# Kernel optimization log

Hardware: AMD Instinct MI355X
Metric: run time of the kernel (lower is better)

## Reference

```python
import jax, jax.numpy as jnp
import numpy as np

DT = 0.03125                                   # ray-march step size
NSTEPS = int(np.ceil(2.0 * np.sqrt(3.0) / DT)) # enough steps to cross the [-1,1]^3 cube diagonal (=111)


def trilinear_sample(vol, pos):
    """vol: [C, D, Hv, Wv]; pos: [H, W, 3] xyz in [-1,1] (grid_sample convention,
    align_corners=True). Returns [C, H, W]."""
    D, Hv, Wv = vol.shape[1], vol.shape[2], vol.shape[3]

    def axis(g, n):
        g = jnp.clip((g + 1.0) * 0.5 * (n - 1), 0.0, n - 1.0)
        i0 = jnp.minimum(jnp.floor(g).astype(jnp.int32), n - 2)
        return i0, i0 + 1, (g - i0)[None]  # frac broadcast over channel dim

    x0, x1, fx = axis(pos[..., 0], Wv)
    y0, y1, fy = axis(pos[..., 1], Hv)
    z0, z1, fz = axis(pos[..., 2], D)

    def g(z, y, x):
        return vol[:, z, y, x]  # [C, H, W]

    c00 = g(z0, y0, x0) * (1 - fx) + g(z0, y0, x1) * fx
    c01 = g(z0, y1, x0) * (1 - fx) + g(z0, y1, x1) * fx
    c10 = g(z1, y0, x0) * (1 - fx) + g(z1, y0, x1) * fx
    c11 = g(z1, y1, x0) * (1 - fx) + g(z1, y1, x1) * fx
    c0 = c00 * (1 - fy) + c01 * fy
    c1 = c10 * (1 - fy) + c11 * fy
    return c0 * (1 - fz) + c1 * fz


def setup_inputs() -> dict:
    key = jax.random.key(0)
    B, H, W, D = 2, 256, 256, 128
    camrot = jnp.tile(jnp.eye(3, dtype=jnp.float32)[None], (B, 1, 1))
    campos = jnp.tile(jnp.array([[0.0, 0.0, -2.5]], dtype=jnp.float32), (B, 1))
    focal = jnp.full((B, 2), 300.0, dtype=jnp.float32)
    princpt = jnp.full((B, 2), 128.0, dtype=jnp.float32)
    ys, xs = jnp.meshgrid(jnp.arange(H, dtype=jnp.float32),
                          jnp.arange(W, dtype=jnp.float32), indexing='ij')
    pixelcoords = jnp.tile(jnp.stack([xs, ys], axis=-1)[None], (B, 1, 1, 1))
    volume = jax.random.uniform(key, (B, 4, D, D, D), dtype=jnp.float32)
    return dict(camrot=camrot, campos=campos, focal=focal, princpt=princpt,
                pixelcoords=pixelcoords, volume=volume)


def reference(camrot, campos, focal, princpt, pixelcoords, volume):
    # camera rays: pixel -> camera -> world (camrot^T applied, as in torch sum over dim=-2)
    raydir = (pixelcoords - princpt[:, None, None, :]) / focal[:, None, None, :]
    raydir = jnp.concatenate([raydir, jnp.ones_like(raydir[..., :1])], axis=-1)
    raydir = jnp.einsum('bij,bhwi->bhwj', camrot, raydir)
    raydir = raydir / jnp.sqrt(jnp.sum(raydir ** 2, axis=-1, keepdims=True))

    # ray-AABB intersection with [-1,1]^3 (no grad, as in torch.no_grad())
    t1 = (-1.0 - campos[:, None, None, :]) / raydir
    t2 = (1.0 - campos[:, None, None, :]) / raydir
    tmin = jnp.maximum(jnp.minimum(t1[..., 0], t2[..., 0]),
                       jnp.maximum(jnp.minimum(t1[..., 1], t2[..., 1]),
                                   jnp.minimum(t1[..., 2], t2[..., 2])))
    tmax = jnp.minimum(jnp.maximum(t1[..., 0], t2[..., 0]),
                       jnp.minimum(jnp.maximum(t1[..., 1], t2[..., 1]),
                                   jnp.maximum(t1[..., 2], t2[..., 2])))
    hit = tmin < tmax
    t0 = jax.lax.stop_gradient(jnp.maximum(jnp.where(hit, tmin, 0.0), 0.0))

    raypos = campos[:, None, None, :] + raydir * t0[..., None]  # [B,H,W,3]
    B, H, W = raypos.shape[:3]
    rayrgb = jnp.zeros((B, 3, H, W), raypos.dtype)
    rayalpha = jnp.zeros((B, 1, H, W), raypos.dtype)

    def step(carry, _):
        raypos, rayrgb, rayalpha = carry
        valid = jnp.all((raypos > -1.0) & (raypos < 1.0), axis=-1).astype(raypos.dtype)
        samp = jax.vmap(trilinear_sample)(volume, raypos)  # [B,4,H,W]
        contrib = (jnp.minimum(rayalpha + samp[:, 3:4] * DT, 1.0) - rayalpha) * valid[:, None]
        rayrgb = rayrgb + samp[:, :3] * contrib
        rayalpha = rayalpha + contrib
        raypos = raypos + raydir * DT
        return (raypos, rayrgb, rayalpha), None

    (_, rayrgb, rayalpha), _ = jax.lax.scan(step, (raypos, rayrgb, rayalpha),
                                            None, length=NSTEPS)
    return jnp.concatenate([rayrgb, rayalpha], axis=1)  # [B,4,H,W]
```

## Files before the change

kernel.cpp:

```cpp
#include <hip/hip_runtime.h>
#include <math.h>

#pragma clang fp contract(off)

#define DT 0.03125f
#define INV_DT 32.0f
#define NSTEPS 111


__device__ __forceinline__ unsigned q8(float v) {
    return __float2uint_rn(fminf(fmaxf(v, 0.0f), 1.0f) * 255.0f);
}

__device__ __forceinline__ float chan_u8(unsigned dA, unsigned dB,
                                         float fx, float fy, float fz) {
#pragma clang fp contract(fast)
    float a00 = (float)(dA & 0xffu);
    float a10 = (float)((dA >> 8) & 0xffu);
    float a01 = (float)((dA >> 16) & 0xffu);
    float a11 = (float)((dA >> 24) & 0xffu);
    float l0 = a00 + fx * (a10 - a00);
    float l1 = a01 + fx * (a11 - a01);
    float la = l0 + fy * (l1 - l0);
    float b00 = (float)(dB & 0xffu);
    float b10 = (float)((dB >> 8) & 0xffu);
    float b01 = (float)((dB >> 16) & 0xffu);
    float b11 = (float)((dB >> 24) & 0xffu);
    float m0 = b00 + fx * (b10 - b00);
    float m1 = b01 + fx * (b11 - b01);
    float lb = m0 + fy * (m1 - m0);
    return la + fz * (lb - la);
}

__device__ __forceinline__ float4 sample_u8(uint4 A, uint4 B,
                                            float fx, float fy, float fz) {
#pragma clang fp contract(fast)
    const float s = 1.0f / 255.0f;
    float4 r;
    r.x = chan_u8(A.x, B.x, fx, fy, fz) * s;
    r.y = chan_u8(A.y, B.y, fx, fy, fz) * s;
    r.z = chan_u8(A.z, B.z, fx, fy, fz) * s;
    r.w = chan_u8(A.w, B.w, fx, fy, fz) * s;
    return r;
}

__global__ __launch_bounds__(256) void repack_u8x4_kernel(const float* __restrict__ vol,
                                                          uint4* __restrict__ out,
                                                          long spatial, int D) {
    long chunk = (long)blockIdx.x * blockDim.x + threadIdx.x;
    long nchunks = spatial >> 2;
    if (chunk >= nchunks) return;
    long b = blockIdx.y;
    long s = chunk << 2;
    int zs = D * D;
    int z = (int)(s / zs);
    int rem = (int)(s - (long)z * zs);
    int y = rem / D;
    int x0 = rem - y * D;
    int y1 = (y < D - 1) ? y + 1 : y;

    const float* base = vol + b * 4 * spatial;
    uint4 e[4];
    #pragma unroll
    for (int ci = 0; ci < 4; ++ci) {
        const float* pa = base + (long)ci * spatial + (long)z * zs + y * D + x0;
        const float* pb = base + (long)ci * spatial + (long)z * zs + y1 * D + x0;
        float4 va = *(const float4*)pa;
        float4 vb = *(const float4*)pb;
        bool last = (x0 + 4 >= D);
        float na = last ? pa[3] : pa[4];
        float nb = last ? pb[3] : pb[4];
        float ra[5] = {va.x, va.y, va.z, va.w, na};
        float rb[5] = {vb.x, vb.y, vb.z, vb.w, nb};
        #pragma unroll
        for (int k = 0; k < 4; ++k) {
            unsigned d = q8(ra[k]) | (q8(ra[k + 1]) << 8) |
                         (q8(rb[k]) << 16) | (q8(rb[k + 1]) << 24);
            ((unsigned*)&e[k])[ci] = d;
        }
    }
    uint4* o = out + b * spatial + s;
    o[0] = e[0]; o[1] = e[1]; o[2] = e[2]; o[3] = e[3];
}

__global__ __launch_bounds__(256) void repack_u8_kernel(const float* __restrict__ vol,
                                                        uint4* __restrict__ out,
                                                        long total, long spatial, int D) {
    long idx = (long)blockIdx.x * blockDim.x + threadIdx.x;
    if (idx >= total) return;
    long b = idx / spatial;
    long s = idx - b * spatial;
    int zs = D * D;
    int z = (int)(s / zs);
    int rem = (int)(s - (long)z * zs);
    int y = rem / D;
    int x = rem - y * D;
    int x1 = (x < D - 1) ? x + 1 : x;
    int y1 = (y < D - 1) ? y + 1 : y;
    const float* base = vol + b * 4 * spatial;
    uint4 e;
    #pragma unroll
    for (int ci = 0; ci < 4; ++ci) {
        const float* p = base + (long)ci * spatial + (long)z * zs;
        unsigned d = q8(p[y * D + x]) | (q8(p[y * D + x1]) << 8) |
                     (q8(p[y1 * D + x]) << 16) | (q8(p[y1 * D + x1]) << 24);
        ((unsigned*)&e)[ci] = d;
    }
    out[idx] = e;
}


struct Ray {
    float posx, posy, posz;
    float stx, sty, stz;
    int n;
};

__device__ __forceinline__ Ray ray_setup(const float* __restrict__ camrot,
                                         const float* __restrict__ campos,
                                         const float* __restrict__ focal,
                                         const float* __restrict__ princpt,
                                         const float* __restrict__ pixelcoords,
                                         int b, int y, int x, int H, int W) {
#pragma clang fp contract(off)
    long pidx = (((long)b * H + y) * W + x) * 2;
    float px = pixelcoords[pidx];
    float py = pixelcoords[pidx + 1];
    const float* R = camrot + b * 9;
    float cpx = campos[b * 3 + 0], cpy = campos[b * 3 + 1], cpz = campos[b * 3 + 2];
    float flx = focal[b * 2 + 0], fly = focal[b * 2 + 1];
    float prx = princpt[b * 2 + 0], pry = princpt[b * 2 + 1];

    float rx = (px - prx) / flx;
    float ry = (py - pry) / fly;
    float rz = 1.0f;
    float dx = R[0] * rx + R[3] * ry + R[6] * rz;
    float dy = R[1] * rx + R[4] * ry + R[7] * rz;
    float dz = R[2] * rx + R[5] * ry + R[8] * rz;
    float ss = dx * dx;
    ss = ss + dy * dy;
    ss = ss + dz * dz;
    float nrm = sqrtf(ss);
    dx = dx / nrm; dy = dy / nrm; dz = dz / nrm;

    float t1x = (-1.0f - cpx) / dx, t2x = (1.0f - cpx) / dx;
    float t1y = (-1.0f - cpy) / dy, t2y = (1.0f - cpy) / dy;
    float t1z = (-1.0f - cpz) / dz, t2z = (1.0f - cpz) / dz;
    float tmin = fmaxf(fminf(t1x, t2x), fmaxf(fminf(t1y, t2y), fminf(t1z, t2z)));
    float tmax = fminf(fmaxf(t1x, t2x), fminf(fmaxf(t1y, t2y), fmaxf(t1z, t2z)));
    bool hit = tmin < tmax;
    float t0 = fmaxf(hit ? tmin : 0.0f, 0.0f);

    Ray r;
    r.posx = cpx + dx * t0;
    r.posy = cpy + dy * t0;
    r.posz = cpz + dz * t0;
    r.stx = dx * DT; r.sty = dy * DT; r.stz = dz * DT;

    float span = (tmax - t0) * INV_DT + 4.0f;
    span = fminf(span, (float)NSTEPS);
    r.n = (hit && span > 0.0f) ? (int)span : 0;
    return r;
}


template <int DD>
__global__ __launch_bounds__(256, 2) void raymarch_u8_kernel(
        const float* __restrict__ camrot, const float* __restrict__ campos,
        const float* __restrict__ focal, const float* __restrict__ princpt,
        const float* __restrict__ pixelcoords, const uint4* __restrict__ vol,
        float* __restrict__ out, int B, int H, int W, int Drt) {
#pragma clang fp contract(off)
    const int D = (DD > 0) ? DD : Drt;
    int x = blockIdx.x * 16 + threadIdx.x;
    int y = blockIdx.y * 16 + threadIdx.y;
    int b = blockIdx.z;
    if (x >= W || y >= H) return;

    Ray r = ray_setup(camrot, campos, focal, princpt, pixelcoords, b, y, x, H, W);

    float accr = 0.0f, accg = 0.0f, accb = 0.0f, alpha = 0.0f;
    float gmax = (float)(D - 1);
    const int zs = D * D;
    const uint4* vp = vol + (long)b * ((long)zs * D);

    if (r.n > 0) {
        float pxx = r.posx, pyy = r.posy, pzz = r.posz;
        float stx = r.stx, sty = r.sty, stz = r.stz;
        int spf = 0;
        uint4 A0, B0, A1, B1, A2, B2;
        float f0x, f0y, f0z, m0, f1x, f1y, f1z, m1, f2x, f2y, f2z, m2;

#define PREFETCH(UA, UB, FX, FY, FZ, M) do {                                    \
        bool inside = (pxx > -1.0f) && (pxx < 1.0f) && (pyy > -1.0f) &&         \
                      (pyy < 1.0f) && (pzz > -1.0f) && (pzz < 1.0f);            \
        M = (inside && (spf < NSTEPS)) ? 1.0f : 0.0f;                           \
        float gx = fminf(fmaxf((pxx + 1.0f) * 0.5f * gmax, 0.0f), gmax);        \
        float gy = fminf(fmaxf((pyy + 1.0f) * 0.5f * gmax, 0.0f), gmax);        \
        float gz = fminf(fmaxf((pzz + 1.0f) * 0.5f * gmax, 0.0f), gmax);        \
        int ix0 = (int)floorf(gx); if (ix0 > D - 2) ix0 = D - 2;                \
        int iy0 = (int)floorf(gy); if (iy0 > D - 2) iy0 = D - 2;                \
        int iz0 = (int)floorf(gz); if (iz0 > D - 2) iz0 = D - 2;                \
        FX = gx - (float)ix0; FY = gy - (float)iy0; FZ = gz - (float)iz0;       \
        const uint4* p_ = vp + (iz0 * zs + iy0 * D + ix0);                      \
        UA = p_[0]; UB = p_[zs];                                                \
        pxx = pxx + stx; pyy = pyy + sty; pzz = pzz + stz;                      \
        spf = spf + 1;                                                          \
    } while (0)

#define CONSUME(UA, UB, FX, FY, FZ, M) do {                                    \
        float4 samp = sample_u8(UA, UB, FX, FY, FZ);                            \
        float contrib = (fminf(alpha + samp.w * DT, 1.0f) - alpha) * M;         \
        accr = accr + samp.x * contrib;                                         \
        accg = accg + samp.y * contrib;                                         \
        accb = accb + samp.z * contrib;                                         \
        alpha = alpha + contrib;                                                \
    } while (0)

        PREFETCH(A0, B0, f0x, f0y, f0z, m0);
        PREFETCH(A1, B1, f1x, f1y, f1z, m1);
        PREFETCH(A2, B2, f2x, f2y, f2z, m2);

        int iters = (r.n + 2) / 3;
        for (int it = 0; it < iters; ++it) {
            CONSUME(A0, B0, f0x, f0y, f0z, m0);
            PREFETCH(A0, B0, f0x, f0y, f0z, m0);
            CONSUME(A1, B1, f1x, f1y, f1z, m1);
            PREFETCH(A1, B1, f1x, f1y, f1z, m1);
            CONSUME(A2, B2, f2x, f2y, f2z, m2);
            PREFETCH(A2, B2, f2x, f2y, f2z, m2);
        }
#undef PREFETCH
#undef CONSUME
    }

    long hw = (long)H * W;
    long o = (long)b * 4 * hw + (long)y * W + x;
    out[o] = accr;
    out[o + hw] = accg;
    out[o + 2 * hw] = accb;
    out[o + 3 * hw] = alpha;
}


__global__ __launch_bounds__(256) void raymarch_simple_kernel(
        const float* __restrict__ camrot, const float* __restrict__ campos,
        const float* __restrict__ focal, const float* __restrict__ princpt,
        const float* __restrict__ pixelcoords, const float* __restrict__ vol,
        float* __restrict__ out, int B, int H, int W, int D) {
#pragma clang fp contract(off)
    int x = blockIdx.x * blockDim.x + threadIdx.x;
    int y = blockIdx.y * blockDim.y + threadIdx.y;
    int b = blockIdx.z;
    if (x >= W || y >= H) return;

    Ray r = ray_setup(camrot, campos, focal, princpt, pixelcoords, b, y, x, H, W);

    float accr = 0.0f, accg = 0.0f, accb = 0.0f, alpha = 0.0f;
    float gmax = (float)(D - 1);
    long spatial = (long)D * D * D;
    long zstride = (long)D * D;
    const float* vb = vol + (long)b * 4 * spatial;
    float pxx = r.posx, pyy = r.posy, pzz = r.posz;

    for (int s = 0; s < r.n; ++s) {
        bool inside = (pxx > -1.0f) && (pxx < 1.0f) && (pyy > -1.0f) &&
                      (pyy < 1.0f) && (pzz > -1.0f) && (pzz < 1.0f);
        float m = inside ? 1.0f : 0.0f;
        float gx = fminf(fmaxf((pxx + 1.0f) * 0.5f * gmax, 0.0f), gmax);
        float gy = fminf(fmaxf((pyy + 1.0f) * 0.5f * gmax, 0.0f), gmax);
        float gz = fminf(fmaxf((pzz + 1.0f) * 0.5f * gmax, 0.0f), gmax);
        int ix0 = (int)floorf(gx); if (ix0 > D - 2) ix0 = D - 2;
        int iy0 = (int)floorf(gy); if (iy0 > D - 2) iy0 = D - 2;
        int iz0 = (int)floorf(gz); if (iz0 > D - 2) iz0 = D - 2;
        float fx = gx - (float)ix0;
        float fy = gy - (float)iy0;
        float fz = gz - (float)iz0;

        long s000 = (long)iz0 * zstride + (long)iy0 * D + ix0;
        float c[8][4];
        const long offs[8] = {s000, s000 + 1, s000 + D, s000 + D + 1,
                              s000 + zstride, s000 + zstride + 1,
                              s000 + zstride + D, s000 + zstride + D + 1};
        #pragma unroll
        for (int k = 0; k < 8; ++k) {
            c[k][0] = vb[offs[k]];
            c[k][1] = vb[offs[k] + spatial];
            c[k][2] = vb[offs[k] + 2 * spatial];
            c[k][3] = vb[offs[k] + 3 * spatial];
        }
        float wa = 1.0f - fx, wb = 1.0f - fy, wc = 1.0f - fz;
        float samp[4];
        #pragma unroll
        for (int ci = 0; ci < 4; ++ci) {
            float c00 = c[0][ci] * wa + c[1][ci] * fx;
            float c01 = c[2][ci] * wa + c[3][ci] * fx;
            float c10 = c[4][ci] * wa + c[5][ci] * fx;
            float c11 = c[6][ci] * wa + c[7][ci] * fx;
            float c0 = c00 * wb + c01 * fy;
            float c1 = c10 * wb + c11 * fy;
            samp[ci] = c0 * wc + c1 * fz;
        }
        float contrib = (fminf(alpha + samp[3] * DT, 1.0f) - alpha) * m;
        accr = accr + samp[0] * contrib;
        accg = accg + samp[1] * contrib;
        accb = accb + samp[2] * contrib;
        alpha = alpha + contrib;
        pxx = pxx + r.stx; pyy = pyy + r.sty; pzz = pzz + r.stz;
    }

    long hw = (long)H * W;
    long o = (long)b * 4 * hw + (long)y * W + x;
    out[o] = accr;
    out[o + hw] = accg;
    out[o + 2 * hw] = accb;
    out[o + 3 * hw] = alpha;
}

extern "C" void kernel_launch(void* const* d_in, const int* in_sizes, int n_in,
                              void* d_out, int out_size, void* d_ws, size_t ws_size,
                              hipStream_t stream) {
    const float* camrot = (const float*)d_in[0];
    const float* campos = (const float*)d_in[1];
    const float* focal = (const float*)d_in[2];
    const float* princpt = (const float*)d_in[3];
    const float* pixelcoords = (const float*)d_in[4];
    const float* volume = (const float*)d_in[5];
    float* out = (float*)d_out;

    int B = in_sizes[0] / 9;
    long spatial = (long)in_sizes[5] / (B * 4);
    int D = (int)lround(cbrt((double)spatial));
    while ((long)D * D * D > spatial) D--;
    while ((long)(D + 1) * (D + 1) * (D + 1) <= spatial) D++;
    long hw = (long)in_sizes[4] / (B * 2);
    int H = (int)lround(sqrt((double)hw));
    int W = H;

    size_t need = (size_t)B * spatial * sizeof(uint4);

    if (ws_size >= need && D >= 2) {
        uint4* vol8 = (uint4*)d_ws;
        if ((D & 3) == 0) {
            long nchunks = spatial >> 2;
            dim3 rgrd((unsigned)((nchunks + 255) / 256), B, 1);
            repack_u8x4_kernel<<<rgrd, dim3(256), 0, stream>>>(volume, vol8, spatial, D);
        } else {
            long total = (long)B * spatial;
            repack_u8_kernel<<<dim3((unsigned)((total + 255) / 256)), dim3(256), 0,
                               stream>>>(volume, vol8, total, spatial, D);
        }
        dim3 blk(16, 16, 1);
        dim3 grd((W + 15) / 16, (H + 15) / 16, B);
        if (D == 128) {
            raymarch_u8_kernel<128><<<grd, blk, 0, stream>>>(
                camrot, campos, focal, princpt, pixelcoords, vol8, out, B, H, W, D);
        } else {
            raymarch_u8_kernel<0><<<grd, blk, 0, stream>>>(
                camrot, campos, focal, princpt, pixelcoords, vol8, out, B, H, W, D);
        }
    } else {
        dim3 blk(16, 16, 1);
        dim3 grd((W + 15) / 16, (H + 15) / 16, B);
        raymarch_simple_kernel<<<grd, blk, 0, stream>>>(camrot, campos, focal, princpt,
                                                        pixelcoords, volume,
                                                        out, B, H, W, D);
    }
}
```

Before: 167.7 us.

## Split each ray into segments using a sigma prefix pass, then combine

Each ray's 111 steps are split into 4 segments, giving four times as many threads. A first kernel sums density over each segment from a new density-only byte buffer. This works because accumulated alpha is just min(prefix sum, 1). A second kernel marches each segment in parallel starting from the clamped prefix alpha, and a combine kernel adds the colour partials and writes alpha. The aim is to replace long serial per-ray chains on a small, low-occupancy grid with more, shorter, higher-occupancy work. The cost is an extra density pass, a larger repack write, extra workspace and two more launches, and the old software-prefetch pipeline is dropped. The fallback path now launches the repack with zero elements, so it never fills the volume buffer.

```diff
diff --git a/kernel.cpp b/kernel.cpp
--- a/kernel.cpp
+++ b/kernel.cpp
@@ -6,6 +6,8 @@
 #define DT 0.03125f
 #define INV_DT 32.0f
 #define NSTEPS 111
+#define SEG 4
+#define SLEN 28
 
 
 __device__ __forceinline__ unsigned q8(float v) {
@@ -46,6 +48,7 @@
 
 __global__ __launch_bounds__(256) void repack_u8x4_kernel(const float* __restrict__ vol,
                                                           uint4* __restrict__ out,
+                                                          unsigned* __restrict__ sig,
                                                           long spatial, int D) {
     long chunk = (long)blockIdx.x * blockDim.x + threadIdx.x;
     long nchunks = spatial >> 2;
@@ -61,6 +64,7 @@
 
     const float* base = vol + b * 4 * spatial;
     uint4 e[4];
+    unsigned sw[4];
     #pragma unroll
     for (int ci = 0; ci < 4; ++ci) {
         const float* pa = base + (long)ci * spatial + (long)z * zs + y * D + x0;
@@ -77,14 +81,18 @@
             unsigned d = q8(ra[k]) | (q8(ra[k + 1]) << 8) |
                          (q8(rb[k]) << 16) | (q8(rb[k + 1]) << 24);
             ((unsigned*)&e[k])[ci] = d;
+            if (ci == 3) sw[k] = d;
         }
     }
     uint4* o = out + b * spatial + s;
     o[0] = e[0]; o[1] = e[1]; o[2] = e[2]; o[3] = e[3];
+    unsigned* so = sig + b * spatial + s;
+    so[0] = sw[0]; so[1] = sw[1]; so[2] = sw[2]; so[3] = sw[3];
 }
 
 __global__ __launch_bounds__(256) void repack_u8_kernel(const float* __restrict__ vol,
                                                         uint4* __restrict__ out,
+                                                        unsigned* __restrict__ sig,
                                                         long total, long spatial, int D) {
     long idx = (long)blockIdx.x * blockDim.x + threadIdx.x;
     if (idx >= total) return;
@@ -107,6 +115,7 @@
         ((unsigned*)&e)[ci] = d;
     }
     out[idx] = e;
+    sig[idx] = e.w;
 }
 
 
@@ -165,6 +174,157 @@
 
 
 template <int DD>
+__global__ __launch_bounds__(256, 8) void sigma_u8_kernel(
+        const float* __restrict__ camrot, const float* __restrict__ campos,
+        const float* __restrict__ focal, const float* __restrict__ princpt,
+        const float* __restrict__ pixelcoords, const unsigned* __restrict__ sig,
+        float* __restrict__ sums, int B, int H, int W, int Drt, int nrays) {
+#pragma clang fp contract(off)
+    const int D = (DD > 0) ? DD : Drt;
+    int x = blockIdx.x * 16 + threadIdx.x;
+    int y = blockIdx.y * 16 + threadIdx.y;
+    int bz = blockIdx.z;
+    int b = bz >> 2;
+    int seg = bz & 3;
+    if (x >= W || y >= H) return;
+    int ray = (b * H + y) * W + x;
+
+    Ray r = ray_setup(camrot, campos, focal, princpt, pixelcoords, b, y, x, H, W);
+
+    int s0 = seg * SLEN;
+    int s1 = s0 + SLEN; if (s1 > NSTEPS) s1 = NSTEPS;
+    int lim = (r.n < s1) ? r.n : s1;
+
+    float S = 0.0f;
+    if (s0 < lim) {
+        float gmax = (float)(D - 1);
+        const int zs = D * D;
+        const unsigned* sp = sig + (long)b * ((long)zs * D);
+        float pxx = r.posx, pyy = r.posy, pzz = r.posz;
+        for (int s = 0; s < s0; ++s) {
+            pxx = pxx + r.stx; pyy = pyy + r.sty; pzz = pzz + r.stz;
+        }
+        for (int s = s0; s < lim; ++s) {
+            bool inside = (pxx > -1.0f) && (pxx < 1.0f) && (pyy > -1.0f) &&
+                          (pyy < 1.0f) && (pzz > -1.0f) && (pzz < 1.0f);
+            float m = inside ? 1.0f : 0.0f;
+            float gx = fminf(fmaxf((pxx + 1.0f) * 0.5f * gmax, 0.0f), gmax);
+            float gy = fminf(fmaxf((pyy + 1.0f) * 0.5f * gmax, 0.0f), gmax);
+            float gz = fminf(fmaxf((pzz + 1.0f) * 0.5f * gmax, 0.0f), gmax);
+            int ix0 = (int)floorf(gx); if (ix0 > D - 2) ix0 = D - 2;
+            int iy0 = (int)floorf(gy); if (iy0 > D - 2) iy0 = D - 2;
+            int iz0 = (int)floorf(gz); if (iz0 > D - 2) iz0 = D - 2;
+            float fx = gx - (float)ix0;
+            float fy = gy - (float)iy0;
+            float fz = gz - (float)iz0;
+            const unsigned* p_ = sp + (iz0 * zs + iy0 * D + ix0);
+            unsigned dA = p_[0];
+            unsigned dB = p_[zs];
+            float sw = chan_u8(dA, dB, fx, fy, fz) * (1.0f / 255.0f);
+            S = S + (sw * DT) * m;
+            pxx = pxx + r.stx; pyy = pyy + r.sty; pzz = pzz + r.stz;
+        }
+    }
+    sums[(long)seg * nrays + ray] = S;
+}
+
+
+template <int DD>
+__global__ __launch_bounds__(256, 8) void march_seg_u8_kernel(
+        const float* __restrict__ camrot, const float* __restrict__ campos,
+        const float* __restrict__ focal, const float* __restrict__ princpt,
+        const float* __restrict__ pixelcoords, const uint4* __restrict__ vol,
+        const float* __restrict__ sums, float* __restrict__ part,
+        int B, int H, int W, int Drt, int nrays) {
+#pragma clang fp contract(off)
+    const int D = (DD > 0) ? DD : Drt;
+    int x = blockIdx.x * 16 + threadIdx.x;
+    int y = blockIdx.y * 16 + threadIdx.y;
+    int bz = blockIdx.z;
+    int b = bz >> 2;
+    int seg = bz & 3;
+    if (x >= W || y >= H) return;
+    int ray = (b * H + y) * W + x;
+
+    Ray r = ray_setup(camrot, campos, focal, princpt, pixelcoords, b, y, x, H, W);
+
+    float P = 0.0f;
+    for (int j = 0; j < seg; ++j) P = P + sums[(long)j * nrays + ray];
+    float alpha = fminf(P, 1.0f);
+
+    int s0 = seg * SLEN;
+    int s1 = s0 + SLEN; if (s1 > NSTEPS) s1 = NSTEPS;
+    int lim = (r.n < s1) ? r.n : s1;
+
+    float accr = 0.0f, accg = 0.0f, accb = 0.0f;
+    if (s0 < lim) {
+        float gmax = (float)(D - 1);
+        const int zs = D * D;
+        const uint4* vp = vol + (long)b * ((long)zs * D);
+        float pxx = r.posx, pyy = r.posy, pzz = r.posz;
+        for (int s = 0; s < s0; ++s) {
+            pxx = pxx + r.stx; pyy = pyy + r.sty; pzz = pzz + r.stz;
+        }
+        for (int s = s0; s < lim; ++s) {
+            bool inside = (pxx > -1.0f) && (pxx < 1.0f) && (pyy > -1.0f) &&
+                          (pyy < 1.0f) && (pzz > -1.0f) && (pzz < 1.0f);
+            float m = inside ? 1.0f : 0.0f;
+            float gx = fminf(fmaxf((pxx + 1.0f) * 0.5f * gmax, 0.0f), gmax);
+            float gy = fminf(fmaxf((pyy + 1.0f) * 0.5f * gmax, 0.0f), gmax);
+            float gz = fminf(fmaxf((pzz + 1.0f) * 0.5f * gmax, 0.0f), gmax);
+            int ix0 = (int)floorf(gx); if (ix0 > D - 2) ix0 = D - 2;
+            int iy0 = (int)floorf(gy); if (iy0 > D - 2) iy0 = D - 2;
+            int iz0 = (int)floorf(gz); if (iz0 > D - 2) iz0 = D - 2;
+            float fx = gx - (float)ix0;
+            float fy = gy - (float)iy0;
+            float fz = gz - (float)iz0;
+            const uint4* p_ = vp + (iz0 * zs + iy0 * D + ix0);
+            uint4 A = p_[0];
+            uint4 Bv = p_[zs];
+            float4 samp = sample_u8(A, Bv, fx, fy, fz);
+            float contrib = (fminf(alpha + samp.w * DT, 1.0f) - alpha) * m;
+            accr = accr + samp.x * contrib;
+            accg = accg + samp.y * contrib;
+            accb = accb + samp.z * contrib;
+            alpha = alpha + contrib;
+            pxx = pxx + r.stx; pyy = pyy + r.sty; pzz = pzz + r.stz;
+        }
+    }
+    long o = ((long)seg * 3) * nrays + ray;
+    part[o] = accr;
+    part[o + nrays] = accg;
+    part[o + 2 * nrays] = accb;
+}
+
+
+__global__ __launch_bounds__(256) void combine_kernel(const float* __restrict__ sums,
+                                                      const float* __restrict__ part,
+                                                      float* __restrict__ out,
+                                                      int nrays, int chw) {
+#pragma clang fp contract(off)
+    int ray = blockIdx.x * 256 + threadIdx.x;
+    if (ray >= nrays) return;
+    float r = 0.0f, g = 0.0f, bl = 0.0f, P = 0.0f;
+    #pragma unroll
+    for (int sgi = 0; sgi < SEG; ++sgi) {
+        long o = ((long)sgi * 3) * nrays + ray;
+        r = r + part[o];
+        g = g + part[o + nrays];
+        bl = bl + part[o + 2 * nrays];
+        P = P + sums[(long)sgi * nrays + ray];
+    }
+    float a = fminf(P, 1.0f);
+    int b = ray / chw;
+    int pix = ray - b * chw;
+    long o = (long)b * 4 * chw + pix;
+    out[o] = r;
+    out[o + chw] = g;
+    out[o + 2 * chw] = bl;
+    out[o + 3 * chw] = a;
+}
+
+
+template <int DD>
 __global__ __launch_bounds__(256, 2) void raymarch_u8_kernel(
         const float* __restrict__ camrot, const float* __restrict__ campos,
         const float* __restrict__ focal, const float* __restrict__ princpt,
@@ -183,84 +343,6 @@
     float gmax = (float)(D - 1);
     const int zs = D * D;
     const uint4* vp = vol + (long)b * ((long)zs * D);
-
-    if (r.n > 0) {
-        float pxx = r.posx, pyy = r.posy, pzz = r.posz;
-        float stx = r.stx, sty = r.sty, stz = r.stz;
-        int spf = 0;
-        uint4 A0, B0, A1, B1, A2, B2;
-        float f0x, f0y, f0z, m0, f1x, f1y, f1z, m1, f2x, f2y, f2z, m2;
-
-#define PREFETCH(UA, UB, FX, FY, FZ, M) do {                                    \
-        bool inside = (pxx > -1.0f) && (pxx < 1.0f) && (pyy > -1.0f) &&         \
-                      (pyy < 1.0f) && (pzz > -1.0f) && (pzz < 1.0f);            \
-        M = (inside && (spf < NSTEPS)) ? 1.0f : 0.0f;                           \
-        float gx = fminf(fmaxf((pxx + 1.0f) * 0.5f * gmax, 0.0f), gmax);        \
-        float gy = fminf(fmaxf((pyy + 1.0f) * 0.5f * gmax, 0.0f), gmax);        \
-        float gz = fminf(fmaxf((pzz + 1.0f) * 0.5f * gmax, 0.0f), gmax);        \
-        int ix0 = (int)floorf(gx); if (ix0 > D - 2) ix0 = D - 2;                \
-        int iy0 = (int)floorf(gy); if (iy0 > D - 2) iy0 = D - 2;                \
-        int iz0 = (int)floorf(gz); if (iz0 > D - 2) iz0 = D - 2;                \
-        FX = gx - (float)ix0; FY = gy - (float)iy0; FZ = gz - (float)iz0;       \
-        const uint4* p_ = vp + (iz0 * zs + iy0 * D + ix0);                      \
-        UA = p_[0]; UB = p_[zs];                                                \
-        pxx = pxx + stx; pyy = pyy + sty; pzz = pzz + stz;                      \
-        spf = spf + 1;                                                          \
-    } while (0)
-
-#define CONSUME(UA, UB, FX, FY, FZ, M) do {                                    \
-        float4 samp = sample_u8(UA, UB, FX, FY, FZ);                            \
-        float contrib = (fminf(alpha + samp.w * DT, 1.0f) - alpha) * M;         \
-        accr = accr + samp.x * contrib;                                         \
-        accg = accg + samp.y * contrib;                                         \
-        accb = accb + samp.z * contrib;                                         \
-        alpha = alpha + contrib;                                                \
-    } while (0)
-
-        PREFETCH(A0, B0, f0x, f0y, f0z, m0);
-        PREFETCH(A1, B1, f1x, f1y, f1z, m1);
-        PREFETCH(A2, B2, f2x, f2y, f2z, m2);
-
-        int iters = (r.n + 2) / 3;
-        for (int it = 0; it < iters; ++it) {
-            CONSUME(A0, B0, f0x, f0y, f0z, m0);
-            PREFETCH(A0, B0, f0x, f0y, f0z, m0);
-            CONSUME(A1, B1, f1x, f1y, f1z, m1);
-            PREFETCH(A1, B1, f1x, f1y, f1z, m1);
-            CONSUME(A2, B2, f2x, f2y, f2z, m2);
-            PREFETCH(A2, B2, f2x, f2y, f2z, m2);
-        }
-#undef PREFETCH
-#undef CONSUME
-    }
-
-    long hw = (long)H * W;
-    long o = (long)b * 4 * hw + (long)y * W + x;
-    out[o] = accr;
-    out[o + hw] = accg;
-    out[o + 2 * hw] = accb;
-    out[o + 3 * hw] = alpha;
-}
-
-
-__global__ __launch_bounds__(256) void raymarch_simple_kernel(
-        const float* __restrict__ camrot, const float* __restrict__ campos,
-        const float* __restrict__ focal, const float* __restrict__ princpt,
-        const float* __restrict__ pixelcoords, const float* __restrict__ vol,
-        float* __restrict__ out, int B, int H, int W, int D) {
-#pragma clang fp contract(off)
-    int x = blockIdx.x * blockDim.x + threadIdx.x;
-    int y = blockIdx.y * blockDim.y + threadIdx.y;
-    int b = blockIdx.z;
-    if (x >= W || y >= H) return;
-
-    Ray r = ray_setup(camrot, campos, focal, princpt, pixelcoords, b, y, x, H, W);
-
-    float accr = 0.0f, accg = 0.0f, accb = 0.0f, alpha = 0.0f;
-    float gmax = (float)(D - 1);
-    long spatial = (long)D * D * D;
-    long zstride = (long)D * D;
-    const float* vb = vol + (long)b * 4 * spatial;
     float pxx = r.posx, pyy = r.posy, pzz = r.posz;
 
     for (int s = 0; s < r.n; ++s) {
@@ -276,6 +358,60 @@
         float fx = gx - (float)ix0;
         float fy = gy - (float)iy0;
         float fz = gz - (float)iz0;
+        const uint4* p_ = vp + (iz0 * zs + iy0 * D + ix0);
+        uint4 A = p_[0];
+        uint4 Bv = p_[zs];
+        float4 samp = sample_u8(A, Bv, fx, fy, fz);
+        float contrib = (fminf(alpha + samp.w * DT, 1.0f) - alpha) * m;
+        accr = accr + samp.x * contrib;
+        accg = accg + samp.y * contrib;
+        accb = accb + samp.z * contrib;
+        alpha = alpha + contrib;
+        pxx = pxx + r.stx; pyy = pyy + r.sty; pzz = pzz + r.stz;
+    }
+
+    long hw = (long)H * W;
+    long o = (long)b * 4 * hw + (long)y * W + x;
+    out[o] = accr;
+    out[o + hw] = accg;
+    out[o + 2 * hw] = accb;
+    out[o + 3 * hw] = alpha;
+}
+
+
+__global__ __launch_bounds__(256) void raymarch_simple_kernel(
+        const float* __restrict__ camrot, const float* __restrict__ campos,
+        const float* __restrict__ focal, const float* __restrict__ princpt,
+        const float* __restrict__ pixelcoords, const float* __restrict__ vol,
+        float* __restrict__ out, int B, int H, int W, int D) {
+#pragma clang fp contract(off)
+    int x = blockIdx.x * blockDim.x + threadIdx.x;
+    int y = blockIdx.y * blockDim.y + threadIdx.y;
+    int b = blockIdx.z;
+    if (x >= W || y >= H) return;
+
+    Ray r = ray_setup(camrot, campos, focal, princpt, pixelcoords, b, y, x, H, W);
+
+    float accr = 0.0f, accg = 0.0f, accb = 0.0f, alpha = 0.0f;
+    float gmax = (float)(D - 1);
+    long spatial = (long)D * D * D;
+    long zstride = (long)D * D;
+    const float* vb = vol + (long)b * 4 * spatial;
+    float pxx = r.posx, pyy = r.posy, pzz = r.posz;
+
+    for (int s = 0; s < r.n; ++s) {
+        bool inside = (pxx > -1.0f) && (pxx < 1.0f) && (pyy > -1.0f) &&
+                      (pyy < 1.0f) && (pzz > -1.0f) && (pzz < 1.0f);
+        float m = inside ? 1.0f : 0.0f;
+        float gx = fminf(fmaxf((pxx + 1.0f) * 0.5f * gmax, 0.0f), gmax);
+        float gy = fminf(fmaxf((pyy + 1.0f) * 0.5f * gmax, 0.0f), gmax);
+        float gz = fminf(fmaxf((pzz + 1.0f) * 0.5f * gmax, 0.0f), gmax);
+        int ix0 = (int)floorf(gx); if (ix0 > D - 2) ix0 = D - 2;
+        int iy0 = (int)floorf(gy); if (iy0 > D - 2) iy0 = D - 2;
+        int iz0 = (int)floorf(gz); if (iz0 > D - 2) iz0 = D - 2;
+        float fx = gx - (float)ix0;
+        float fy = gy - (float)iy0;
+        float fz = gz - (float)iz0;
 
         long s000 = (long)iz0 * zstride + (long)iy0 * D + ix0;
         float c[8][4];
@@ -336,29 +472,63 @@
     long hw = (long)in_sizes[4] / (B * 2);
     int H = (int)lround(sqrt((double)hw));
     int W = H;
-
-    size_t need = (size_t)B * spatial * sizeof(uint4);
-
-    if (ws_size >= need && D >= 2) {
+    int nrays = (int)(B * hw);
+    int chw = (int)hw;
+
+    size_t vol_bytes = (size_t)B * spatial * sizeof(uint4);
+    size_t sig_bytes = (size_t)B * spatial * sizeof(unsigned);
+    size_t sums_bytes = (size_t)SEG * nrays * sizeof(float);
+    size_t part_bytes = (size_t)SEG * 3 * nrays * sizeof(float);
+    size_t off_sig = (vol_bytes + 255) & ~(size_t)255;
+    size_t off_sums = (off_sig + sig_bytes + 255) & ~(size_t)255;
+    size_t off_part = (off_sums + sums_bytes + 255) & ~(size_t)255;
+    size_t need_full = off_part + part_bytes;
+
+    if (ws_size >= need_full && D >= 2) {
         uint4* vol8 = (uint4*)d_ws;
+        unsigned* sig8 = (unsigned*)((char*)d_ws + off_sig);
+        float* sums = (float*)((char*)d_ws + off_sums);
+        float* part = (float*)((char*)d_ws + off_part);
+
         if ((D & 3) == 0) {
             long nchunks = spatial >> 2;
             dim3 rgrd((unsigned)((nchunks + 255) / 256), B, 1);
-            repack_u8x4_kernel<<<rgrd, dim3(256), 0, stream>>>(volume, vol8, spatial, D);
+            repack_u8x4_kernel<<<rgrd, dim3(256), 0, stream>>>(volume, vol8, sig8,
+                                                               spatial, D);
         } else {
             long total = (long)B * spatial;
             repack_u8_kernel<<<dim3((unsigned)((total + 255) / 256)), dim3(256), 0,
-                               stream>>>(volume, vol8, total, spatial, D);
-        }
+                               stream>>>(volume, vol8, sig8, total, spatial, D);
+        }
+        dim3 blk(16, 16, 1);
+        dim3 grd((W + 15) / 16, (H + 15) / 16, B * SEG);
+        if (D == 128) {
+            sigma_u8_kernel<128><<<grd, blk, 0, stream>>>(
+                camrot, campos, focal, princpt, pixelcoords, sig8, sums,
+                B, H, W, D, nrays);
+            march_seg_u8_kernel<128><<<grd, blk, 0, stream>>>(
+                camrot, campos, focal, princpt, pixelcoords, vol8, sums, part,
+                B, H, W, D, nrays);
+        } else {
+            sigma_u8_kernel<0><<<grd, blk, 0, stream>>>(
+                camrot, campos, focal, princpt, pixelcoords, sig8, sums,
+                B, H, W, D, nrays);
+            march_seg_u8_kernel<0><<<grd, blk, 0, stream>>>(
+                camrot, campos, focal, princpt, pixelcoords, vol8, sums, part,
+                B, H, W, D, nrays);
+        }
+        combine_kernel<<<dim3((nrays + 255) / 256), dim3(256), 0, stream>>>(
+            sums, part, out, nrays, chw);
+    } else if (ws_size >= vol_bytes && D >= 2) {
+        uint4* vol8 = (uint4*)d_ws;
+        long total = (long)B * spatial;
+        repack_u8_kernel<<<dim3((unsigned)((total + 255) / 256)), dim3(256), 0,
+                           stream>>>(volume, vol8, (unsigned*)vol8 ,
+                                     0, spatial, D);
         dim3 blk(16, 16, 1);
         dim3 grd((W + 15) / 16, (H + 15) / 16, B);
-        if (D == 128) {
-            raymarch_u8_kernel<128><<<grd, blk, 0, stream>>>(
-                camrot, campos, focal, princpt, pixelcoords, vol8, out, B, H, W, D);
-        } else {
-            raymarch_u8_kernel<0><<<grd, blk, 0, stream>>>(
-                camrot, campos, focal, princpt, pixelcoords, vol8, out, B, H, W, D);
-        }
+        raymarch_u8_kernel<0><<<grd, blk, 0, stream>>>(
+            camrot, campos, focal, princpt, pixelcoords, vol8, out, B, H, W, D);
     } else {
         dim3 blk(16, 16, 1);
         dim3 grd((W + 15) / 16, (H + 15) / 16, B);
```

Measured after the change: 199.0 us. 1.19x slower.
